# Kernel optimization log

Measured on AMD Instinct MI355X. Metric: run time of the kernel, lower is better.

## Reference

```python
import jax, jax.numpy as jnp
import numpy as np

HIDDEN = 7168
NH = 32
DQ = 1536
DKV = 512
DH = 128   # up_projected_head_size
DR = 64    # rope_head_size
ROPE_BASE = 10000.0


def rms_norm(x, g):
    eps = jnp.finfo(x.dtype).eps
    var = jnp.mean(x * x, axis=-1, keepdims=True)
    return x * jax.lax.rsqrt(var + eps) * g


def apply_rope(x):
    # x: [B, H, S, D] -- rotate-half RoPE with cos/sin built as cat(freqs,freqs)
    S, D = x.shape[-2], x.shape[-1]
    inv_freq = 1.0 / (ROPE_BASE ** (jnp.arange(0, D, 2, dtype=jnp.float32) / D))
    t = jnp.arange(S, dtype=jnp.float32)
    freqs = jnp.outer(t, inv_freq)                 # [S, D/2]
    emb = jnp.concatenate([freqs, freqs], axis=-1)  # [S, D]
    cos, sin = jnp.cos(emb), jnp.sin(emb)
    x1, x2 = x[..., : D // 2], x[..., D // 2:]
    rotated = jnp.concatenate([-x2, x1], axis=-1)
    return x * cos + rotated * sin


def setup_inputs() -> dict:
    key = jax.random.key(0)
    ks = jax.random.split(key, 8)
    s = 0.02
    return {
        "hidden_states": jax.random.normal(ks[0], (1, 2048, HIDDEN), jnp.float32),
        "W_dq": jax.random.normal(ks[1], (HIDDEN, DQ), jnp.float32) * s,
        "g_q": jnp.ones((DQ,), jnp.float32),
        "W_uq": jax.random.normal(ks[2], (DQ, NH * (DH + DR)), jnp.float32) * s,
        "W_dkv": jax.random.normal(ks[3], (HIDDEN, DKV + DR), jnp.float32) * s,
        "g_kv": jnp.ones((DKV,), jnp.float32),
        "W_ukv": jax.random.normal(ks[4], (DKV, NH * 2 * DH), jnp.float32) * s,
        "W_o": jax.random.normal(ks[5], (NH * DH, HIDDEN), jnp.float32) * s,
    }


def reference(hidden_states, W_dq, g_q, W_uq, W_dkv, g_kv, W_ukv, W_o):
    B, S, _ = hidden_states.shape
    # Q path: down-proj -> RMSNorm -> up-proj -> split nope/rope parts
    c_q = hidden_states @ W_dq                                   # [B,S,DQ]
    qcr = (rms_norm(c_q, g_q) @ W_uq).reshape(B, S, NH, DH + DR)
    qcr = qcr.transpose(0, 2, 1, 3)                              # [B,NH,S,DH+DR]
    q_c, q_r = qcr[..., :DH], qcr[..., DH:]
    # KV path: joint down-proj for compressed latent + shared MQA rope key
    ckv_kr = hidden_states @ W_dkv                               # [B,S,DKV+DR]
    c_kv, k_r = ckv_kr[..., :DKV], ckv_kr[..., DKV:]
    k_r = k_r[:, None, :, :]                                     # [B,1,S,DR]
    kv = (rms_norm(c_kv, g_kv) @ W_ukv).reshape(B, S, NH, 2 * DH)
    kv = kv.transpose(0, 2, 1, 3)                                # [B,NH,S,2*DH]
    k_c, v = kv[..., :DH], kv[..., DH:]
    # partial RoPE
    q_r = apply_rope(q_r)
    k_r = apply_rope(k_r)
    q = jnp.concatenate([q_c, q_r], axis=-1)                     # [B,NH,S,DH+DR]
    k = jnp.concatenate([k_c, jnp.broadcast_to(k_r, (B, NH, S, DR))], axis=-1)
    # non-causal SDPA, scale = 1/sqrt(q head dim)
    scale = 1.0 / np.sqrt(DH + DR)
    scores = jnp.einsum("bhqd,bhkd->bhqk", q, k) * scale
    attn = jax.nn.softmax(scores, axis=-1)
    o = jnp.einsum("bhqk,bhkd->bhqd", attn, v)                   # [B,NH,S,DH]
    o = o.transpose(0, 2, 1, 3).reshape(B, S, NH * DH)
    return o @ W_o
```

## Files before the change

### kernel.cpp

```cpp
#include <hip/hip_runtime.h>
#include <hip/hip_bf16.h>
#include <math.h>

#define HIDDEN 7168
#define NH 32
#define DQ 1536
#define DKV 512
#define DH 128
#define DR 64
#define SEQ 2048
#define DKVP 640
#define NQKV 2176

typedef unsigned short u16;
typedef __bf16 bf16_t;
typedef bf16_t bf16x8 __attribute__((ext_vector_type(8)));
typedef float f32x4 __attribute__((ext_vector_type(4)));

__device__ __forceinline__ float bf2f(u16 h) {
    union { unsigned u; float f; } q; q.u = ((unsigned)h) << 16; return q.f;
}
__device__ __forceinline__ u16 f2bf(float x) {
    union { float f; unsigned u; } q; q.f = x;
    unsigned r = q.u + 0x7fffu + ((q.u >> 16) & 1u);
    return (u16)(r >> 16);
}

template <typename CT>
__global__ __launch_bounds__(256) void gemm_bt(
    const u16* __restrict__ A, const u16* __restrict__ B, CT* __restrict__ C,
    int K, int lda, int ldb, int ldc, long sA, long sB, long sC)
{
    __shared__ u16 As[128 * 32];
    __shared__ u16 Bs[128 * 32];
    A += (long)blockIdx.z * sA;
    B += (long)blockIdx.z * sB;
    C += (long)blockIdx.z * sC;

    const int t = threadIdx.x;
    const int w = t >> 6, lane = t & 63;
    const int lane15 = lane & 15, quad = lane >> 4;
    const int brow = blockIdx.y * 128, bcol = blockIdx.x * 128;
    const int wrow = (w >> 1) * 64, wcol = (w & 1) * 64;

    f32x4 acc[4][4] = {};

    for (int k0 = 0; k0 < K; k0 += 32) {
#pragma unroll
        for (int i = 0; i < 2; ++i) {
            int chunk = i * 256 + t;
            int row = chunk >> 2;
            int kc = (chunk & 3) * 8;
            const u16* ga = A + (long)(brow + row) * lda + k0 + kc;
            const u16* gb = B + (long)(bcol + row) * ldb + k0 + kc;
            u16* la = As + (i * 256 + w * 64) * 8;
            u16* lb = Bs + (i * 256 + w * 64) * 8;
            __builtin_amdgcn_global_load_lds(
                (const __attribute__((address_space(1))) void*)ga,
                (__attribute__((address_space(3))) void*)la, 16, 0, 0);
            __builtin_amdgcn_global_load_lds(
                (const __attribute__((address_space(1))) void*)gb,
                (__attribute__((address_space(3))) void*)lb, 16, 0, 0);
        }
        __syncthreads();

        bf16x8 af[4], bfr[4];
#pragma unroll
        for (int mi = 0; mi < 4; ++mi)
            af[mi] = *(const bf16x8*)(As + (wrow + mi * 16 + lane15) * 32 + quad * 8);
#pragma unroll
        for (int ni = 0; ni < 4; ++ni)
            bfr[ni] = *(const bf16x8*)(Bs + (wcol + ni * 16 + lane15) * 32 + quad * 8);
#pragma unroll
        for (int mi = 0; mi < 4; ++mi)
#pragma unroll
            for (int ni = 0; ni < 4; ++ni)
                acc[mi][ni] = __builtin_amdgcn_mfma_f32_16x16x32_bf16(
                    af[mi], bfr[ni], acc[mi][ni], 0, 0, 0);
        __syncthreads();
    }

#pragma unroll
    for (int mi = 0; mi < 4; ++mi) {
#pragma unroll
        for (int ni = 0; ni < 4; ++ni) {
            int r0 = brow + wrow + mi * 16 + quad * 4;
            int cc = bcol + wcol + ni * 16 + lane15;
#pragma unroll
            for (int r = 0; r < 4; ++r) {
                float v = acc[mi][ni][r];
                if constexpr (sizeof(CT) == 2) C[(long)(r0 + r) * ldc + cc] = f2bf(v);
                else                           C[(long)(r0 + r) * ldc + cc] = v;
            }
        }
    }
}

__global__ __launch_bounds__(256, 2) void flash_attn(
    const u16* __restrict__ qb, const u16* __restrict__ kb,
    const u16* __restrict__ vT, u16* __restrict__ ob, float scale)
{
    __shared__ u16 Ks[64 * 200];
    __shared__ u16 Vs[128 * 72];
    __shared__ u16 Ps[4 * 32 * 72];

    const int t = threadIdx.x;
    const int w = t >> 6, lane = t & 63;
    const int lane15 = lane & 15, quad = lane >> 4;
    const int h = blockIdx.y;
    const int q0 = blockIdx.x * 128 + w * 32;
    u16* Psw = Ps + w * 32 * 72;

    bf16x8 Qf[2][6];
#pragma unroll
    for (int qt = 0; qt < 2; ++qt)
#pragma unroll
        for (int kc = 0; kc < 6; ++kc)
            Qf[qt][kc] = *(const bf16x8*)(
                qb + (long)(h * SEQ + q0 + qt * 16 + lane15) * 192 + kc * 32 + quad * 8);

    f32x4 O[8][2] = {};
    float mst[2] = { -3.0e38f, -3.0e38f }, lst[2] = { 0.f, 0.f };

    bf16x8 Kpf[6], Vpf[4];
    auto load_tiles = [&](int kt) {
#pragma unroll
        for (int i = 0; i < 6; ++i) {
            int chunk = i * 256 + t;
            int row = chunk / 24, c8 = (chunk % 24) * 8;
            Kpf[i] = *(const bf16x8*)(kb + (long)(h * SEQ + kt * 64 + row) * 192 + c8);
        }
#pragma unroll
        for (int i = 0; i < 4; ++i) {
            int chunk = i * 256 + t;
            int dh = chunk >> 3, c8 = (chunk & 7) * 8;
            Vpf[i] = *(const bf16x8*)(vT + (long)(h * 128 + dh) * SEQ + kt * 64 + c8);
        }
    };
    auto store_tiles = [&]() {
#pragma unroll
        for (int i = 0; i < 6; ++i) {
            int chunk = i * 256 + t;
            int row = chunk / 24, c8 = (chunk % 24) * 8;
            *(bf16x8*)(Ks + row * 200 + c8) = Kpf[i];
        }
#pragma unroll
        for (int i = 0; i < 4; ++i) {
            int chunk = i * 256 + t;
            int dh = chunk >> 3, c8 = (chunk & 7) * 8;
            *(bf16x8*)(Vs + dh * 72 + c8) = Vpf[i];
        }
    };

    load_tiles(0);
    store_tiles();
    __syncthreads();

    for (int kt = 0; kt < SEQ / 64; ++kt) {
        load_tiles(kt + 1 < SEQ / 64 ? kt + 1 : kt);

        f32x4 St[4][2] = {};
#pragma unroll
        for (int kc = 0; kc < 6; ++kc) {
            bf16x8 Kf[4];
#pragma unroll
            for (int k4 = 0; k4 < 4; ++k4)
                Kf[k4] = *(const bf16x8*)(Ks + (k4 * 16 + lane15) * 200 + kc * 32 + quad * 8);
#pragma unroll
            for (int k4 = 0; k4 < 4; ++k4)
#pragma unroll
                for (int qt = 0; qt < 2; ++qt)
                    St[k4][qt] = __builtin_amdgcn_mfma_f32_16x16x32_bf16(
                        Kf[k4], Qf[qt][kc], St[k4][qt], 0, 0, 0);
        }

#pragma unroll
        for (int qt = 0; qt < 2; ++qt) {
            float rm = St[0][qt][0];
#pragma unroll
            for (int k4 = 0; k4 < 4; ++k4)
#pragma unroll
                for (int r = 0; r < 4; ++r) rm = fmaxf(rm, St[k4][qt][r]);
            rm = fmaxf(rm, __shfl_xor(rm, 16, 64));
            rm = fmaxf(rm, __shfl_xor(rm, 32, 64));
            rm *= scale;
            float mnew = fmaxf(mst[qt], rm);
            float alpha = __expf(mst[qt] - mnew);
            mst[qt] = mnew;
            float rs = 0.f;
#pragma unroll
            for (int k4 = 0; k4 < 4; ++k4)
#pragma unroll
                for (int r = 0; r < 4; ++r) {
                    float pv = __expf(St[k4][qt][r] * scale - mnew);
                    St[k4][qt][r] = pv; rs += pv;
                }
            rs += __shfl_xor(rs, 16, 64);
            rs += __shfl_xor(rs, 32, 64);
            lst[qt] = lst[qt] * alpha + rs;
#pragma unroll
            for (int dt = 0; dt < 8; ++dt)
#pragma unroll
                for (int r = 0; r < 4; ++r) O[dt][qt][r] *= alpha;
        }

#pragma unroll
        for (int qt = 0; qt < 2; ++qt)
#pragma unroll
            for (int k4 = 0; k4 < 4; ++k4) {
                ushort4 pk;
                pk.x = f2bf(St[k4][qt][0]); pk.y = f2bf(St[k4][qt][1]);
                pk.z = f2bf(St[k4][qt][2]); pk.w = f2bf(St[k4][qt][3]);
                *(ushort4*)(Psw + (qt * 16 + lane15) * 72 + k4 * 16 + quad * 4) = pk;
            }

#pragma unroll
        for (int kc2 = 0; kc2 < 2; ++kc2) {
            bf16x8 Pf[2], Vf[8];
#pragma unroll
            for (int qt = 0; qt < 2; ++qt)
                Pf[qt] = *(const bf16x8*)(Psw + (qt * 16 + lane15) * 72 + kc2 * 32 + quad * 8);
#pragma unroll
            for (int dt = 0; dt < 8; ++dt)
                Vf[dt] = *(const bf16x8*)(Vs + (dt * 16 + lane15) * 72 + kc2 * 32 + quad * 8);
#pragma unroll
            for (int dt = 0; dt < 8; ++dt)
#pragma unroll
                for (int qt = 0; qt < 2; ++qt)
                    O[dt][qt] = __builtin_amdgcn_mfma_f32_16x16x32_bf16(
                        Vf[dt], Pf[qt], O[dt][qt], 0, 0, 0);
        }
        __syncthreads();
        store_tiles();
        __syncthreads();
    }

#pragma unroll
    for (int qt = 0; qt < 2; ++qt) {
        float inv = 1.f / lst[qt];
        int s = q0 + qt * 16 + lane15;
#pragma unroll
        for (int dt = 0; dt < 8; ++dt) {
            ushort4 ov;
            ov.x = f2bf(O[dt][qt][0] * inv); ov.y = f2bf(O[dt][qt][1] * inv);
            ov.z = f2bf(O[dt][qt][2] * inv); ov.w = f2bf(O[dt][qt][3] * inv);
            *(ushort4*)(ob + (long)s * 4096 + h * 128 + dt * 16 + quad * 4) = ov;
        }
    }
}

__global__ void cast_bf16_k(const float* __restrict__ in, u16* __restrict__ out, long n)
{
    long i = ((long)blockIdx.x * 256 + threadIdx.x) * 4;
    if (i >= n) return;
    float4 v = *(const float4*)(in + i);
    ushort4 o;
    o.x = f2bf(v.x); o.y = f2bf(v.y); o.z = f2bf(v.z); o.w = f2bf(v.w);
    *(ushort4*)(out + i) = o;
}

__global__ void transpose_cast(const float* __restrict__ in, u16* __restrict__ out,
                               int K, int N, int Npad)
{
    __shared__ float tile[32][33];
    int n0 = blockIdx.x * 32, k0 = blockIdx.y * 32;
    int tx = threadIdx.x, ty = threadIdx.y;
#pragma unroll
    for (int i = 0; i < 32; i += 8) {
        int k = k0 + ty + i, n = n0 + tx;
        tile[ty + i][tx] = (n < N) ? in[(long)k * N + n] : 0.f;
    }
    __syncthreads();
#pragma unroll
    for (int i = 0; i < 32; i += 8) {
        int n = n0 + ty + i, k = k0 + tx;
        out[(long)n * K + k] = f2bf(tile[tx][ty + i]);
    }
}

__global__ __launch_bounds__(256) void rmsnorm_k(
    const u16* __restrict__ in, const float* __restrict__ g,
    u16* __restrict__ out, int C, int ldin)
{
    const int row = blockIdx.x;
    const u16* x = in + (long)row * ldin;
    float ss = 0.f;
    for (int c = threadIdx.x; c < C; c += 256) { float v = bf2f(x[c]); ss += v * v; }
#pragma unroll
    for (int off = 32; off; off >>= 1) ss += __shfl_down(ss, off, 64);
    __shared__ float red[4];
    if ((threadIdx.x & 63) == 0) red[threadIdx.x >> 6] = ss;
    __syncthreads();
    float tot = red[0] + red[1] + red[2] + red[3];
    float r = rsqrtf(tot / (float)C + 1.1920929e-07f);
    for (int c = threadIdx.x; c < C; c += 256)
        out[(long)row * C + c] = f2bf(bf2f(x[c]) * r * g[c]);
}

__global__ void rope_tab_k(float* __restrict__ ct, float* __restrict__ st)
{
    int idx = blockIdx.x * 256 + threadIdx.x;
    int s = idx >> 5, j = idx & 31;
    float invf = powf(10000.f, -(float)(2 * j) / 64.f);
    float fr = (float)s * invf;
    float sn, cs; sincosf(fr, &sn, &cs);
    ct[idx] = cs; st[idx] = sn;
}

__device__ __forceinline__ float rope_val(const u16* src, int i, int s,
                                          const float* ct, const float* st)
{
    int j = i & 31;
    float cs = ct[s * 32 + j], sn = st[s * 32 + j];
    float x = bf2f(src[i]);
    float xo = (i < 32) ? bf2f(src[i + 32]) : bf2f(src[i - 32]);
    return (i < 32) ? (x * cs - xo * sn) : (x * cs + xo * sn);
}

__global__ void build_q_k(const u16* __restrict__ qcr, u16* __restrict__ q,
                          const float* __restrict__ ct, const float* __restrict__ st)
{
    int s = blockIdx.x, h = blockIdx.y, d = threadIdx.x;
    const u16* src = qcr + ((long)s * NH + h) * 192;
    float val = (d < 128) ? bf2f(src[d]) : rope_val(src + 128, d - 128, s, ct, st);
    q[((long)h * SEQ + s) * 192 + d] = f2bf(val);
}

__global__ void build_k_k(const u16* __restrict__ kv, const u16* __restrict__ ropebuf,
                          int ldrope, u16* __restrict__ kbuf,
                          const float* __restrict__ ct, const float* __restrict__ st)
{
    int s = blockIdx.x, h = blockIdx.y, d = threadIdx.x;
    float val = (d < 128) ? bf2f(kv[(long)s * 8192 + h * 256 + d])
                          : rope_val(ropebuf + (long)s * ldrope, d - 128, s, ct, st);
    kbuf[((long)h * SEQ + s) * 192 + d] = f2bf(val);
}

__global__ void build_vT_k(const u16* __restrict__ kv, u16* __restrict__ vT)
{
    __shared__ u16 tile[32][33];
    int s0 = blockIdx.x * 32, d0 = blockIdx.y * 32, h = blockIdx.z;
    int tx = threadIdx.x, ty = threadIdx.y;
#pragma unroll
    for (int i = 0; i < 32; i += 8)
        tile[ty + i][tx] = kv[(long)(s0 + ty + i) * 8192 + h * 256 + 128 + d0 + tx];
    __syncthreads();
#pragma unroll
    for (int i = 0; i < 32; i += 8)
        vT[((long)h * 128 + d0 + ty + i) * SEQ + s0 + tx] = tile[tx][ty + i];
}

extern "C" void kernel_launch(void* const* d_in, const int* in_sizes, int n_in,
                              void* d_out, int out_size, void* d_ws, size_t ws_size,
                              hipStream_t stream)
{
    const float* hidden = (const float*)d_in[0];
    const float* W_dq   = (const float*)d_in[1];
    const float* g_q    = (const float*)d_in[2];
    const float* W_uq   = (const float*)d_in[3];
    const float* W_dkv  = (const float*)d_in[4];
    const float* g_kv   = (const float*)d_in[5];
    const float* W_ukv  = (const float*)d_in[6];
    const float* W_o    = (const float*)d_in[7];
    float* out = (float*)d_out;

    char* p = (char*)d_ws;
    auto alloc = [&](size_t bytes) {
        char* r = p; p += (bytes + 255) & ~(size_t)255; return r;
    };
    u16* hbf   = (u16*)alloc((size_t)SEQ * HIDDEN * 2);
    u16* WTqkv = (u16*)alloc((size_t)NQKV * HIDDEN * 2);
    u16* WTuq  = (u16*)alloc((size_t)6144 * DQ * 2);
    u16* WTukv = (u16*)alloc((size_t)8192 * DKV * 2);
    u16* WTo   = (u16*)alloc((size_t)HIDDEN * 4096 * 2);
    u16* cqc   = (u16*)alloc((size_t)SEQ * NQKV * 2);
    u16* nq    = (u16*)alloc((size_t)SEQ * DQ * 2);
    u16* qcr   = (u16*)alloc((size_t)SEQ * 6144 * 2);
    u16* nkv   = (u16*)alloc((size_t)SEQ * DKV * 2);
    u16* kvb   = (u16*)alloc((size_t)SEQ * 8192 * 2);
    u16* qb    = (u16*)alloc((size_t)NH * SEQ * 192 * 2);
    u16* kb    = (u16*)alloc((size_t)NH * SEQ * 192 * 2);
    u16* vT    = (u16*)alloc((size_t)NH * 128 * SEQ * 2);
    u16* ob    = (u16*)alloc((size_t)SEQ * 4096 * 2);
    float* ct  = (float*)alloc((size_t)SEQ * 32 * 4);
    float* st  = (float*)alloc((size_t)SEQ * 32 * 4);
    (void)in_sizes; (void)n_in; (void)out_size; (void)ws_size;

    rope_tab_k<<<(SEQ * 32) / 256, 256, 0, stream>>>(ct, st);
    cast_bf16_k<<<((long)SEQ * HIDDEN) / 1024, 256, 0, stream>>>(hidden, hbf, (long)SEQ * HIDDEN);
    transpose_cast<<<dim3(DQ / 32, HIDDEN / 32), dim3(32, 8), 0, stream>>>(W_dq, WTqkv, HIDDEN, DQ, DQ);
    transpose_cast<<<dim3(DKVP / 32, HIDDEN / 32), dim3(32, 8), 0, stream>>>(
        W_dkv, WTqkv + (size_t)DQ * HIDDEN, HIDDEN, 576, DKVP);
    transpose_cast<<<dim3(6144 / 32, DQ / 32), dim3(32, 8), 0, stream>>>(W_uq, WTuq, DQ, 6144, 6144);
    transpose_cast<<<dim3(8192 / 32, DKV / 32), dim3(32, 8), 0, stream>>>(W_ukv, WTukv, DKV, 8192, 8192);
    transpose_cast<<<dim3(HIDDEN / 32, 4096 / 32), dim3(32, 8), 0, stream>>>(W_o, WTo, 4096, HIDDEN, HIDDEN);

    gemm_bt<u16><<<dim3(NQKV / 128, SEQ / 128), 256, 0, stream>>>(
        hbf, WTqkv, cqc, HIDDEN, HIDDEN, HIDDEN, NQKV, 0, 0, 0);
    rmsnorm_k<<<SEQ, 256, 0, stream>>>(cqc, g_q, nq, DQ, NQKV);
    rmsnorm_k<<<SEQ, 256, 0, stream>>>(cqc + DQ, g_kv, nkv, DKV, NQKV);

    gemm_bt<u16><<<dim3(6144 / 128, SEQ / 128), 256, 0, stream>>>(
        nq, WTuq, qcr, DQ, DQ, DQ, 6144, 0, 0, 0);
    gemm_bt<u16><<<dim3(8192 / 128, SEQ / 128), 256, 0, stream>>>(
        nkv, WTukv, kvb, DKV, DKV, DKV, 8192, 0, 0, 0);

    build_q_k<<<dim3(SEQ, NH), 192, 0, stream>>>(qcr, qb, ct, st);
    build_k_k<<<dim3(SEQ, NH), 192, 0, stream>>>(kvb, cqc + DQ + DKV, NQKV, kb, ct, st);
    build_vT_k<<<dim3(SEQ / 32, 4, NH), dim3(32, 8), 0, stream>>>(kvb, vT);

    const float scale = 0.07216878364870322f;
    flash_attn<<<dim3(SEQ / 128, NH), 256, 0, stream>>>(qb, kb, vT, ob, scale);

    gemm_bt<float><<<dim3(HIDDEN / 128, SEQ / 128), 256, 0, stream>>>(
        ob, WTo, out, 4096, 4096, 4096, HIDDEN, 0, 0, 0);
}
```

Baseline: 993.6 us.

## Add 256x256-tile GEMM with 4-stage direct-to-LDS pipeline for up and output projections

Adds a new GEMM kernel with 256x256 output tiles, 512 threads and a 4-deep ring of LDS buffers filled via global_load_lds. Waits use explicit vmcnt counts, and the grid is remapped in an XCD-aware order. The kernel replaces the 128x128 gemm_bt for the Q/KV up-projections and the output projection. The aim is more data reuse per tile and loads that overlap with MFMA work. The LDS layout is unpadded, so it risks bank conflicts, and the large tiles give fewer workgroups on the smaller GEMMs.

```diff
diff --git a/kernel.cpp b/kernel.cpp
--- a/kernel.cpp
+++ b/kernel.cpp
@@ -91,6 +91,110 @@
                 float v = acc[mi][ni][r];
                 if constexpr (sizeof(CT) == 2) C[(long)(r0 + r) * ldc + cc] = f2bf(v);
                 else                           C[(long)(r0 + r) * ldc + cc] = v;
+            }
+        }
+    }
+}
+
+template <typename CT>
+__global__ __launch_bounds__(512, 2) void gemm256(
+    const u16* __restrict__ A, const u16* __restrict__ B, CT* __restrict__ C,
+    int K, int lda, int ldb, int ldc, int nx)
+{
+    __shared__ u16 lds[4 * 16384];
+    const int t = threadIdx.x;
+    const int lane = t & 63;
+    const int w = t >> 6;
+    const int lane15 = lane & 15, quad = lane >> 4;
+    const int wm = w >> 2, wn = w & 3;
+
+    int nwg = gridDim.x, wg = blockIdx.x, tile = wg;
+    if ((nwg & 7) == 0) { int q = nwg >> 3; tile = (wg & 7) * q + (wg >> 3); }
+    const int bx = tile % nx, by = tile / nx;
+    const long brow = (long)by * 256, bcol = (long)bx * 256;
+
+    const u16* gsrc[4];
+    int loff[4];
+#pragma unroll
+    for (int j = 0; j < 2; ++j) {
+        int c = j * 512 + t;
+        int row = c >> 2, k8 = (c & 3) * 8;
+        gsrc[j]     = A + (brow + row) * lda + k8;
+        gsrc[j + 2] = B + (bcol + row) * ldb + k8;
+        loff[j]     = c * 8;
+        loff[j + 2] = 8192 + c * 8;
+    }
+
+    const int NT = K >> 5;
+    auto stage = [&](int tt) {
+        u16* sb = lds + (tt & 3) * 16384;
+        int ko = tt * 32;
+#pragma unroll
+        for (int j = 0; j < 4; ++j)
+            __builtin_amdgcn_global_load_lds(
+                (const __attribute__((address_space(1))) void*)(gsrc[j] + ko),
+                (__attribute__((address_space(3))) void*)(sb + loff[j]), 16, 0, 0);
+    };
+
+    f32x4 acc[8][4] = {};
+    const int aoff = (wm * 128 + lane15) * 32 + quad * 8;
+    const int boff = 8192 + (wn * 64 + lane15) * 32 + quad * 8;
+
+    stage(0); stage(1); stage(2);
+
+    for (int T = 0; T < NT; ++T) {
+        int rem = NT - 1 - T;
+        if (rem >= 2)      asm volatile("s_waitcnt vmcnt(8)" ::: "memory");
+        else if (rem == 1) asm volatile("s_waitcnt vmcnt(4)" ::: "memory");
+        else               asm volatile("s_waitcnt vmcnt(0)" ::: "memory");
+        __builtin_amdgcn_s_barrier();
+        __builtin_amdgcn_sched_barrier(0);
+        if (T + 3 < NT) stage(T + 3);
+
+        const u16* sb = lds + (T & 3) * 16384;
+        bf16x8 bfr[4], af[8];
+#pragma unroll
+        for (int ni = 0; ni < 4; ++ni)
+            bfr[ni] = *(const bf16x8*)(sb + boff + ni * 512);
+#pragma unroll
+        for (int mi = 0; mi < 4; ++mi)
+            af[mi] = *(const bf16x8*)(sb + aoff + mi * 512);
+        __builtin_amdgcn_s_setprio(1);
+#pragma unroll
+        for (int mi = 0; mi < 4; ++mi)
+#pragma unroll
+            for (int ni = 0; ni < 4; ++ni)
+                acc[mi][ni] = __builtin_amdgcn_mfma_f32_16x16x32_bf16(
+                    af[mi], bfr[ni], acc[mi][ni], 0, 0, 0);
+        __builtin_amdgcn_s_setprio(0);
+#pragma unroll
+        for (int mi = 4; mi < 8; ++mi)
+            af[mi] = *(const bf16x8*)(sb + aoff + mi * 512);
+        __builtin_amdgcn_s_setprio(1);
+#pragma unroll
+        for (int mi = 4; mi < 8; ++mi)
+#pragma unroll
+            for (int ni = 0; ni < 4; ++ni)
+                acc[mi][ni] = __builtin_amdgcn_mfma_f32_16x16x32_bf16(
+                    af[mi], bfr[ni], acc[mi][ni], 0, 0, 0);
+        __builtin_amdgcn_s_setprio(0);
+        asm volatile("s_waitcnt lgkmcnt(0)" ::: "memory");
+        __builtin_amdgcn_sched_barrier(0);
+    }
+
+    const long crow0 = brow + wm * 128 + quad * 4;
+    const long ccol0 = bcol + wn * 64 + lane15;
+#pragma unroll
+    for (int mi = 0; mi < 8; ++mi) {
+#pragma unroll
+        for (int ni = 0; ni < 4; ++ni) {
+            long r0 = crow0 + mi * 16;
+            long cc = ccol0 + ni * 16;
+#pragma unroll
+            for (int r = 0; r < 4; ++r) {
+                float v = acc[mi][ni][r];
+                if constexpr (sizeof(CT) == 2) C[(r0 + r) * ldc + cc] = f2bf(v);
+                else                           C[(r0 + r) * ldc + cc] = v;
             }
         }
     }
@@ -400,10 +504,10 @@
     rmsnorm_k<<<SEQ, 256, 0, stream>>>(cqc, g_q, nq, DQ, NQKV);
     rmsnorm_k<<<SEQ, 256, 0, stream>>>(cqc + DQ, g_kv, nkv, DKV, NQKV);
 
-    gemm_bt<u16><<<dim3(6144 / 128, SEQ / 128), 256, 0, stream>>>(
-        nq, WTuq, qcr, DQ, DQ, DQ, 6144, 0, 0, 0);
-    gemm_bt<u16><<<dim3(8192 / 128, SEQ / 128), 256, 0, stream>>>(
-        nkv, WTukv, kvb, DKV, DKV, DKV, 8192, 0, 0, 0);
+    gemm256<u16><<<dim3((SEQ / 256) * (6144 / 256)), 512, 0, stream>>>(
+        nq, WTuq, qcr, DQ, DQ, DQ, 6144, 6144 / 256);
+    gemm256<u16><<<dim3((SEQ / 256) * (8192 / 256)), 512, 0, stream>>>(
+        nkv, WTukv, kvb, DKV, DKV, DKV, 8192, 8192 / 256);
 
     build_q_k<<<dim3(SEQ, NH), 192, 0, stream>>>(qcr, qb, ct, st);
     build_k_k<<<dim3(SEQ, NH), 192, 0, stream>>>(kvb, cqc + DQ + DKV, NQKV, kb, ct, st);
@@ -412,6 +516,6 @@
     const float scale = 0.07216878364870322f;
     flash_attn<<<dim3(SEQ / 128, NH), 256, 0, stream>>>(qb, kb, vT, ob, scale);
 
-    gemm_bt<float><<<dim3(HIDDEN / 128, SEQ / 128), 256, 0, stream>>>(
-        ob, WTo, out, 4096, 4096, 4096, HIDDEN, 0, 0, 0);
-}
+    gemm256<float><<<dim3((SEQ / 256) * (HIDDEN / 256)), 512, 0, stream>>>(
+        ob, WTo, out, 4096, 4096, 4096, HIDDEN, HIDDEN / 256);
+}
```

Measured after the change: 887.8 us. -10.6%, faster.
